# Kernel optimization log

Measured on AMD Instinct MI355X. Metric: run time of the kernel, lower is better.

## Reference

```python
import jax, jax.numpy as jnp
import numpy as np

N = 8192
IN_DIM = 128
OUT_DIM = 128


def setup_inputs() -> dict:
    key = jax.random.key(0)
    ks = jax.random.split(key, 8)
    x = jax.random.normal(ks[0], (N, IN_DIM), dtype=jnp.float32)
    support0 = jax.random.normal(ks[1], (N, N), dtype=jnp.float32) / np.sqrt(N)
    support1 = jax.random.normal(ks[2], (N, N), dtype=jnp.float32) / np.sqrt(N)
    support2 = jax.random.normal(ks[3], (N, N), dtype=jnp.float32) / np.sqrt(N)
    # glorot-initialized dense projection weight
    limit = np.sqrt(6.0 / (IN_DIM + OUT_DIM))
    W = jax.random.uniform(ks[4], (IN_DIM, OUT_DIM), minval=-limit, maxval=limit, dtype=jnp.float32)
    # depthwise per-channel scales (random instead of ones/zeros init for nontrivial test)
    sd0 = jax.random.normal(ks[5], (IN_DIM,), dtype=jnp.float32)
    sd1 = jax.random.normal(ks[6], (IN_DIM,), dtype=jnp.float32)
    sd2 = jax.random.normal(ks[7], (IN_DIM,), dtype=jnp.float32)
    return {"x": x, "support0": support0, "support1": support1, "support2": support2,
            "W": W, "sd0": sd0, "sd1": sd1, "sd2": sd2}


def reference(x, support0, support1, support2, W, sd0, sd1, sd2):
    # depthwise path: aggregate with each support, scale per-channel, sum, project, relu
    agg = (support0 @ x) * sd0 + (support1 @ x) * sd1 + (support2 @ x) * sd2  # [N, IN_DIM]
    out = agg @ W  # [N, OUT_DIM]
    return jax.nn.relu(out)
```

## Files before the change

kernel.cpp:

```cpp
#include <hip/hip_runtime.h>
#include <hip/hip_bf16.h>

typedef __bf16 bf16x8 __attribute__((ext_vector_type(8)));
typedef float f32x4 __attribute__((ext_vector_type(4)));
typedef unsigned short ushort_t;

#define NN 8192
#define DD 128
#define KTOT 24576
#define SPLITS 8
#define KSPLIT 3072
#define BM 128

__global__ __launch_bounds__(256) void bprep_kernel(
    const float* __restrict__ x, const float* __restrict__ W,
    const float* __restrict__ sd0, const float* __restrict__ sd1,
    const float* __restrict__ sd2, ushort_t* __restrict__ Bws)
{
    const int tid = threadIdx.x;
    const int n  = tid & 127;
    const int rg = tid >> 7;
    const int r0 = blockIdx.x * 16;
    const int sup = r0 >> 13;
    const float* sd = (sup == 0) ? sd0 : ((sup == 1) ? sd1 : sd2);
    const int xrow0 = (r0 & (NN - 1)) + rg * 8;

    float acc[8];
#pragma unroll
    for (int i = 0; i < 8; ++i) acc[i] = 0.f;

    for (int c = 0; c < DD; ++c) {
        float wv = sd[c] * W[c * DD + n];
#pragma unroll
        for (int i = 0; i < 8; ++i)
            acc[i] = fmaf(x[(size_t)(xrow0 + i) * DD + c], wv, acc[i]);
    }

    const int t = n >> 4;
    const int nlo = n & 15;
#pragma unroll
    for (int i = 0; i < 8; ++i) {
        int r   = r0 + rg * 8 + i;
        int cc  = r >> 5;
        int rem = r & 31;
        int hi  = rem >> 3;
        int j   = rem & 7;
        int ll  = hi * 16 + nlo;
        size_t idx = (((size_t)cc * 8 + t) * 64 + ll) * 8 + j;
        __bf16 b = (__bf16)acc[i];
        ushort_t u;
        __builtin_memcpy(&u, &b, sizeof(u));
        Bws[idx] = u;
    }
}

__global__ __launch_bounds__(256, 2) void spmm_kernel(
    const float* __restrict__ s0, const float* __restrict__ s1,
    const float* __restrict__ s2, const ushort_t* __restrict__ Bws,
    float* __restrict__ out)
{
    const int lane  = threadIdx.x & 63;
    const int wave  = threadIdx.x >> 6;
    const int split = blockIdx.x & (SPLITS - 1);
    const int mblk  = blockIdx.x >> 3;
    const int kbase = split * KSPLIT;
    const int m15   = lane & 15;
    const int q     = lane >> 4;
    const int row0  = mblk * BM + wave * 32;

    f32x4 acc[2][8];
#pragma unroll
    for (int ms = 0; ms < 2; ++ms)
#pragma unroll
        for (int t = 0; t < 8; ++t)
            acc[ms][t] = (f32x4){0.f, 0.f, 0.f, 0.f};

    const bf16x8* __restrict__ Bv = reinterpret_cast<const bf16x8*>(Bws);
    const int nsub = KSPLIT / 32;
    const int cg0  = kbase >> 5;

#pragma unroll 2
    for (int c = 0; c < nsub; ++c) {
        const int kg  = kbase + c * 32;
        const int sup = kg >> 13;
        const float* sp = (sup == 0) ? s0 : ((sup == 1) ? s1 : s2);
        const int koff = (kg & (NN - 1)) + q * 8;

        bf16x8 af[2];
#pragma unroll
        for (int ms = 0; ms < 2; ++ms) {
            const float* ap = sp + (size_t)(row0 + ms * 16 + m15) * NN + koff;
            float4 f0 = *reinterpret_cast<const float4*>(ap);
            float4 f1 = *reinterpret_cast<const float4*>(ap + 4);
            bf16x8 a;
            a[0] = (__bf16)f0.x; a[1] = (__bf16)f0.y;
            a[2] = (__bf16)f0.z; a[3] = (__bf16)f0.w;
            a[4] = (__bf16)f1.x; a[5] = (__bf16)f1.y;
            a[6] = (__bf16)f1.z; a[7] = (__bf16)f1.w;
            af[ms] = a;
        }

        const bf16x8* bp = Bv + (size_t)(cg0 + c) * 8 * 64 + lane;
#pragma unroll
        for (int t = 0; t < 8; ++t) {
            bf16x8 bf = bp[(size_t)t * 64];
            acc[0][t] = __builtin_amdgcn_mfma_f32_16x16x32_bf16(af[0], bf, acc[0][t], 0, 0, 0);
            acc[1][t] = __builtin_amdgcn_mfma_f32_16x16x32_bf16(af[1], bf, acc[1][t], 0, 0, 0);
        }
    }

#pragma unroll
    for (int ms = 0; ms < 2; ++ms)
#pragma unroll
        for (int t = 0; t < 8; ++t)
#pragma unroll
            for (int r = 0; r < 4; ++r) {
                int row = row0 + ms * 16 + q * 4 + r;
                int col = t * 16 + m15;
                atomicAdd(out + (size_t)row * DD + col, acc[ms][t][r]);
            }
}

__global__ __launch_bounds__(256) void relu_kernel(float4* __restrict__ out)
{
    int i = blockIdx.x * 256 + threadIdx.x;
    float4 v = out[i];
    v.x = fmaxf(v.x, 0.f);
    v.y = fmaxf(v.y, 0.f);
    v.z = fmaxf(v.z, 0.f);
    v.w = fmaxf(v.w, 0.f);
    out[i] = v;
}

extern "C" void kernel_launch(void* const* d_in, const int* in_sizes, int n_in,
                              void* d_out, int out_size, void* d_ws, size_t ws_size,
                              hipStream_t stream)
{
    (void)in_sizes; (void)n_in; (void)ws_size;
    const float* x   = (const float*)d_in[0];
    const float* s0  = (const float*)d_in[1];
    const float* s1  = (const float*)d_in[2];
    const float* s2  = (const float*)d_in[3];
    const float* W   = (const float*)d_in[4];
    const float* sd0 = (const float*)d_in[5];
    const float* sd1 = (const float*)d_in[6];
    const float* sd2 = (const float*)d_in[7];
    float* out = (float*)d_out;
    ushort_t* Bws = (ushort_t*)d_ws;

    hipMemsetAsync(d_out, 0, (size_t)out_size * sizeof(float), stream);
    bprep_kernel<<<KTOT / 16, 256, 0, stream>>>(x, W, sd0, sd1, sd2, Bws);
    spmm_kernel<<<(NN / BM) * SPLITS, 256, 0, stream>>>(s0, s1, s2, Bws, out);
    relu_kernel<<<out_size / 1024, 256, 0, stream>>>((float4*)d_out);
}
```

Baseline: 839.4 us.

## Stage A tiles via async global-to-LDS double buffering, double split-K, fuse zeroing

The spmm kernel now loads fp32 support tiles into swizzled, double-buffered LDS with global_load_lds, so the next K-step's fetch overlaps MFMA work on the current one. The split-K count doubles to 16 with a different split-to-block mapping, and launch bounds now ask for higher occupancy. The output memset is folded into the bprep kernel, and bprep's inner loop is vectorised with float4 loads. The aim is to hide memory latency on the bandwidth-bound 805MB fp32 support read, at the cost of more atomics and a barrier per step.

```diff
diff --git a/kernel.cpp b/kernel.cpp
--- a/kernel.cpp
+++ b/kernel.cpp
@@ -8,16 +8,27 @@
 #define NN 8192
 #define DD 128
 #define KTOT 24576
-#define SPLITS 8
-#define KSPLIT 3072
+#define SPLITS 16
+#define KSPLIT 1536
+#define NSTEP 48
 #define BM 128
+
+typedef __attribute__((address_space(3))) unsigned int as3_u32;
+typedef const __attribute__((address_space(1))) unsigned int as1_u32;
 
 __global__ __launch_bounds__(256) void bprep_kernel(
     const float* __restrict__ x, const float* __restrict__ W,
     const float* __restrict__ sd0, const float* __restrict__ sd1,
-    const float* __restrict__ sd2, ushort_t* __restrict__ Bws)
+    const float* __restrict__ sd2, ushort_t* __restrict__ Bws,
+    float4* __restrict__ outz, int nz4)
 {
     const int tid = threadIdx.x;
+
+    {
+        int zi = blockIdx.x * 256 + tid;
+        if (zi < nz4) outz[zi] = make_float4(0.f, 0.f, 0.f, 0.f);
+    }
+
     const int n  = tid & 127;
     const int rg = tid >> 7;
     const int r0 = blockIdx.x * 16;
@@ -29,11 +40,20 @@
 #pragma unroll
     for (int i = 0; i < 8; ++i) acc[i] = 0.f;
 
-    for (int c = 0; c < DD; ++c) {
-        float wv = sd[c] * W[c * DD + n];
-#pragma unroll
-        for (int i = 0; i < 8; ++i)
-            acc[i] = fmaf(x[(size_t)(xrow0 + i) * DD + c], wv, acc[i]);
+    for (int c = 0; c < DD; c += 4) {
+        float4 s4 = *reinterpret_cast<const float4*>(sd + c);
+        float wv0 = s4.x * W[(c + 0) * DD + n];
+        float wv1 = s4.y * W[(c + 1) * DD + n];
+        float wv2 = s4.z * W[(c + 2) * DD + n];
+        float wv3 = s4.w * W[(c + 3) * DD + n];
+#pragma unroll
+        for (int i = 0; i < 8; ++i) {
+            float4 xv = *reinterpret_cast<const float4*>(&x[(size_t)(xrow0 + i) * DD + c]);
+            acc[i] = fmaf(xv.x, wv0, acc[i]);
+            acc[i] = fmaf(xv.y, wv1, acc[i]);
+            acc[i] = fmaf(xv.z, wv2, acc[i]);
+            acc[i] = fmaf(xv.w, wv3, acc[i]);
+        }
     }
 
     const int t = n >> 4;
@@ -54,19 +74,41 @@
     }
 }
 
-__global__ __launch_bounds__(256, 2) void spmm_kernel(
+__global__ __launch_bounds__(256, 4) void spmm_kernel(
     const float* __restrict__ s0, const float* __restrict__ s1,
     const float* __restrict__ s2, const ushort_t* __restrict__ Bws,
     float* __restrict__ out)
 {
-    const int lane  = threadIdx.x & 63;
-    const int wave  = threadIdx.x >> 6;
-    const int split = blockIdx.x & (SPLITS - 1);
-    const int mblk  = blockIdx.x >> 3;
+    __shared__ float Alds[2][BM * 32];
+
+    const int tid  = threadIdx.x;
+    const int lane = tid & 63;
+    const int wave = tid >> 6;
+    const int bid  = blockIdx.x;
+    const int split = ((bid & 7) << 1) | ((bid >> 3) & 1);
+    const int mblk  = bid >> 4;
     const int kbase = split * KSPLIT;
     const int m15   = lane & 15;
     const int q     = lane >> 4;
-    const int row0  = mblk * BM + wave * 32;
+    const int mrow0 = mblk * BM;
+    const int rloc  = wave * 32;
+
+    int srow[4], sq16[4];
+#pragma unroll
+    for (int jj = 0; jj < 4; ++jj) {
+        int u = jj * 256 + tid;
+        srow[jj] = u >> 3;
+        sq16[jj] = (u & 7) ^ (srow[jj] & 7);
+    }
+    const int dunit0 = wave * 64;
+
+    int rdu[2][2];
+#pragma unroll
+    for (int ms = 0; ms < 2; ++ms) {
+        int row_l = rloc + ms * 16 + m15;
+        rdu[ms][0] = row_l * 8 + ((q * 2)     ^ (row_l & 7));
+        rdu[ms][1] = row_l * 8 + ((q * 2 + 1) ^ (row_l & 7));
+    }
 
     f32x4 acc[2][8];
 #pragma unroll
@@ -76,37 +118,47 @@
             acc[ms][t] = (f32x4){0.f, 0.f, 0.f, 0.f};
 
     const bf16x8* __restrict__ Bv = reinterpret_cast<const bf16x8*>(Bws);
-    const int nsub = KSPLIT / 32;
-    const int cg0  = kbase >> 5;
-
-#pragma unroll 2
-    for (int c = 0; c < nsub; ++c) {
-        const int kg  = kbase + c * 32;
-        const int sup = kg >> 13;
-        const float* sp = (sup == 0) ? s0 : ((sup == 1) ? s1 : s2);
-        const int koff = (kg & (NN - 1)) + q * 8;
+    const int cg0 = kbase >> 5;
+
+    auto stage = [&](int buf, int c) {
+        const int kg = kbase + c * 32;
+        const float* sp = (kg < NN) ? s0 : ((kg < 2 * NN) ? s1 : s2);
+        const int kk = kg & (NN - 1);
+#pragma unroll
+        for (int jj = 0; jj < 4; ++jj) {
+            const float* src = sp + (size_t)(mrow0 + srow[jj]) * NN + (kk + sq16[jj] * 4);
+            float* dst = &Alds[buf][(size_t)(jj * 256 + dunit0) * 4];
+            __builtin_amdgcn_global_load_lds((as1_u32*)src, (as3_u32*)dst, 16, 0, 0);
+        }
+    };
+
+    stage(0, 0);
+    int cur = 0;
+    for (int c = 0; c < NSTEP; ++c) {
+        __syncthreads();
+        if (c + 1 < NSTEP) stage(cur ^ 1, c + 1);
 
         bf16x8 af[2];
 #pragma unroll
         for (int ms = 0; ms < 2; ++ms) {
-            const float* ap = sp + (size_t)(row0 + ms * 16 + m15) * NN + koff;
-            float4 f0 = *reinterpret_cast<const float4*>(ap);
-            float4 f1 = *reinterpret_cast<const float4*>(ap + 4);
+            f32x4 f0 = *reinterpret_cast<const f32x4*>(&Alds[cur][rdu[ms][0] * 4]);
+            f32x4 f1 = *reinterpret_cast<const f32x4*>(&Alds[cur][rdu[ms][1] * 4]);
             bf16x8 a;
-            a[0] = (__bf16)f0.x; a[1] = (__bf16)f0.y;
-            a[2] = (__bf16)f0.z; a[3] = (__bf16)f0.w;
-            a[4] = (__bf16)f1.x; a[5] = (__bf16)f1.y;
-            a[6] = (__bf16)f1.z; a[7] = (__bf16)f1.w;
+            a[0] = (__bf16)f0[0]; a[1] = (__bf16)f0[1];
+            a[2] = (__bf16)f0[2]; a[3] = (__bf16)f0[3];
+            a[4] = (__bf16)f1[0]; a[5] = (__bf16)f1[1];
+            a[6] = (__bf16)f1[2]; a[7] = (__bf16)f1[3];
             af[ms] = a;
         }
 
-        const bf16x8* bp = Bv + (size_t)(cg0 + c) * 8 * 64 + lane;
+        const bf16x8* bp = Bv + (size_t)(cg0 + c) * 512 + lane;
 #pragma unroll
         for (int t = 0; t < 8; ++t) {
             bf16x8 bf = bp[(size_t)t * 64];
             acc[0][t] = __builtin_amdgcn_mfma_f32_16x16x32_bf16(af[0], bf, acc[0][t], 0, 0, 0);
             acc[1][t] = __builtin_amdgcn_mfma_f32_16x16x32_bf16(af[1], bf, acc[1][t], 0, 0, 0);
         }
+        cur ^= 1;
     }
 
 #pragma unroll
@@ -115,7 +167,7 @@
         for (int t = 0; t < 8; ++t)
 #pragma unroll
             for (int r = 0; r < 4; ++r) {
-                int row = row0 + ms * 16 + q * 4 + r;
+                int row = mrow0 + rloc + ms * 16 + q * 4 + r;
                 int col = t * 16 + m15;
                 atomicAdd(out + (size_t)row * DD + col, acc[ms][t][r]);
             }
@@ -148,8 +200,8 @@
     float* out = (float*)d_out;
     ushort_t* Bws = (ushort_t*)d_ws;
 
-    hipMemsetAsync(d_out, 0, (size_t)out_size * sizeof(float), stream);
-    bprep_kernel<<<KTOT / 16, 256, 0, stream>>>(x, W, sd0, sd1, sd2, Bws);
+    bprep_kernel<<<KTOT / 16, 256, 0, stream>>>(x, W, sd0, sd1, sd2, Bws,
+                                                (float4*)d_out, out_size / 4);
     spmm_kernel<<<(NN / BM) * SPLITS, 256, 0, stream>>>(s0, s1, s2, Bws, out);
     relu_kernel<<<out_size / 1024, 256, 0, stream>>>((float4*)d_out);
 }
```

Measured after the change: 870.1 us. 3.7% more time.
